# Performance work log

Hardware: AMD Instinct MI355X
Metric: run time of the kernel (lower is better)

The kernel has to match this reference:

```python
import jax, jax.numpy as jnp
import numpy as np

N_NODES = 50000
N_EDGES = 800000
D_IN = 64
D_OUT = 64


def setup_inputs() -> dict:
    key = jax.random.key(0)
    k1, k2, k3 = jax.random.split(key, 3)
    x = jax.random.normal(k1, (N_NODES, D_IN), dtype=jnp.float32)
    edge_index = jax.random.randint(k2, (2, N_EDGES), 0, N_NODES, dtype=jnp.int64)
    # xavier_uniform for weight [in, out]
    limit = np.sqrt(6.0 / (D_IN + D_OUT)).astype(np.float32)
    weight = jax.random.uniform(k3, (D_IN, D_OUT), dtype=jnp.float32, minval=-limit, maxval=limit)
    bias = jnp.zeros((D_OUT,), dtype=jnp.float32)
    return {"x": x, "edge_index": edge_index, "weight": weight, "bias": bias}


def reference(x, edge_index, weight, bias):
    n = x.shape[0]
    # add self loops
    loops = jnp.arange(n, dtype=edge_index.dtype)
    row = jnp.concatenate([edge_index[0], loops])  # [E+N]
    col = jnp.concatenate([edge_index[1], loops])  # [E+N]
    # degree over row (as in torch_geometric degree(row, N))
    deg = jax.ops.segment_sum(jnp.ones_like(row, dtype=x.dtype), row, num_segments=n)
    deg_inv_sqrt = jnp.where(deg > 0, jax.lax.rsqrt(deg), jnp.zeros_like(deg))
    norm = deg_inv_sqrt[row] * deg_inv_sqrt[col]  # [E+N]
    h = x @ weight  # [N, D_OUT]
    # gather-scale-scatter: out[col] += h[row] * norm
    out = jax.ops.segment_sum(h[row] * norm[:, None], col, num_segments=n)
    return out + bias
```

## Files before the change

kernel.cpp:

```cpp
#include <hip/hip_runtime.h>
#include <hip/hip_bf16.h>


constexpr int N_NODES = 50000;
constexpr int N_EDGES = 800000;
constexpr int D = 64;
constexpr int NB_SCAN = (N_NODES + 255) / 256;

constexpr int B_SLICE = 64;
constexpr int SLICE = N_EDGES / B_SLICE;
constexpr int PACK8 = N_NODES / 4;
constexpr int QUAR = N_NODES / 4;

static __device__ __forceinline__ unsigned short f2bf(float f) {
    unsigned u = __float_as_uint(f);
    unsigned r = (u + 0x7fffu + ((u >> 16) & 1u)) >> 16;
    return (unsigned short)r;
}
static __device__ __forceinline__ float bf2f(unsigned short s) {
    return __uint_as_float((unsigned)s << 16);
}


__global__ __launch_bounds__(1024) void hist_priv_kernel(const int* __restrict__ ei,
                                                         unsigned* __restrict__ bh) {
    __shared__ unsigned loc[PACK8];
    int b = blockIdx.x;
    int s = b & (B_SLICE - 1);
    const int* arr = (b < B_SLICE) ? ei : ei + N_EDGES;
    for (int w = threadIdx.x; w < PACK8; w += 1024) loc[w] = 0;
    __syncthreads();
    const int* p = arr + s * SLICE;
    for (int i = threadIdx.x; i < SLICE; i += 1024) {
        int k = p[i];
        atomicAdd(&loc[k >> 2], 1u << (8 * (k & 3)));
    }
    __syncthreads();
    unsigned* dst = bh + (size_t)b * PACK8;
    for (int w = threadIdx.x; w < PACK8; w += 1024) dst[w] = loc[w];
}

__global__ __launch_bounds__(256) void reduce_scan_kernel(const unsigned* __restrict__ bh,
                                                          float* __restrict__ dis,
                                                          int* __restrict__ cnt,
                                                          int* __restrict__ offs_local,
                                                          int* __restrict__ partials) {
    int t = threadIdx.x;
    int i = blockIdx.x * 256 + t;
    unsigned c = 0;
    if (i < N_NODES) {
        int w = i >> 2;
        unsigned sh = 8 * (i & 3);
        const unsigned* prow = bh + w;
        const unsigned* pcol = bh + (size_t)B_SLICE * PACK8 + w;
        unsigned dl = 0, cl = 0;
        unsigned vr[16];
#pragma unroll
        for (int g = 0; g < 4; ++g) {
#pragma unroll
            for (int k = 0; k < 16; ++k) vr[k] = prow[(size_t)(g * 16 + k) * PACK8];
#pragma unroll
            for (int k = 0; k < 16; ++k) dl += (vr[k] >> sh) & 0xffu;
        }
#pragma unroll
        for (int g = 0; g < 4; ++g) {
#pragma unroll
            for (int k = 0; k < 16; ++k) vr[k] = pcol[(size_t)(g * 16 + k) * PACK8];
#pragma unroll
            for (int k = 0; k < 16; ++k) cl += (vr[k] >> sh) & 0xffu;
        }
        c = cl;
        dis[i] = rsqrtf((float)dl + 1.0f);
        cnt[i] = (int)cl;
    }
    __shared__ int s[256];
    s[t] = (int)c;
    __syncthreads();
    for (int d = 1; d < 256; d <<= 1) {
        int u = (t >= d) ? s[t - d] : 0;
        __syncthreads();
        s[t] += u;
        __syncthreads();
    }
    if (i < N_NODES) offs_local[i] = s[t] - (int)c;
    if (t == 255) partials[blockIdx.x] = s[t];
}

__global__ __launch_bounds__(256) void colscan_kernel(const unsigned* __restrict__ bh,
                                                      const int* __restrict__ offs_local,
                                                      const int* __restrict__ partials,
                                                      int* __restrict__ offs,
                                                      unsigned char* __restrict__ bs8) {
    __shared__ int pref[256];
    int t = threadIdx.x;
    int v = (t < NB_SCAN) ? partials[t] : 0;
    pref[t] = v;
    __syncthreads();
    for (int d = 1; d < 256; d <<= 1) {
        int u = (t >= d) ? pref[t - d] : 0;
        __syncthreads();
        pref[t] += u;
        __syncthreads();
    }
    int ex = pref[t] - v;
    __syncthreads();
    pref[t] = ex;
    __syncthreads();

    int i = blockIdx.x * 256 + t;
    if (i >= N_NODES) return;
    offs[i] = pref[blockIdx.x] + offs_local[i];

    int w = i >> 2;
    unsigned sh = 8 * (i & 3);
    const unsigned* src = bh + (size_t)B_SLICE * PACK8 + w;
    unsigned vals[B_SLICE];
#pragma unroll
    for (int b = 0; b < B_SLICE; ++b) vals[b] = src[(size_t)b * PACK8];
    unsigned rel = 0;
#pragma unroll
    for (int b = 0; b < B_SLICE; ++b) {
        bs8[(size_t)b * N_NODES + i] = (unsigned char)rel;
        rel += (vals[b] >> sh) & 0xffu;
    }
}

__global__ __launch_bounds__(1024) void bucket_det_kernel(const int* __restrict__ ei,
                                                          const int* __restrict__ offs,
                                                          const unsigned char* __restrict__ bs8,
                                                          int* __restrict__ csr) {
    __shared__ unsigned pos[QUAR];
    int s = blockIdx.x >> 2;
    int q = blockIdx.x & 3;
    int c0 = q * QUAR;
    const int* offq = offs + c0;
    const unsigned char* relq = bs8 + (size_t)s * N_NODES + c0;
    for (int w = threadIdx.x; w < QUAR; w += 1024)
        pos[w] = (unsigned)offq[w] + relq[w];
    __syncthreads();
    const int* row = ei + s * SLICE;
    const int* col = ei + N_EDGES + s * SLICE;
    for (int i = threadIdx.x; i < SLICE; i += 1024) {
        int c = col[i];
        if (c >= c0 && c < c0 + QUAR) {
            unsigned p = atomicAdd(&pos[c - c0], 1u);
            csr[p] = row[i];
        }
    }
}


__global__ void hist_kernel(const int* __restrict__ row, const int* __restrict__ col,
                            int* __restrict__ degi, int* __restrict__ cnt) {
    int e = blockIdx.x * blockDim.x + threadIdx.x;
    if (e < N_EDGES) {
        atomicAdd(&degi[row[e]], 1);
        atomicAdd(&cnt[col[e]], 1);
    }
}

__global__ void dis_kernel(int* __restrict__ degi) {
    int i = blockIdx.x * blockDim.x + threadIdx.x;
    if (i < N_NODES) {
        float d = (float)degi[i] + 1.0f;
        ((float*)degi)[i] = rsqrtf(d);
    }
}

__global__ void bucket_kernel(const int* __restrict__ row, const int* __restrict__ col,
                              const int* __restrict__ offs, int* __restrict__ cur,
                              int* __restrict__ csr) {
    int e = blockIdx.x * blockDim.x + threadIdx.x;
    if (e < N_EDGES) {
        int c = col[e];
        int pos = offs[c] + atomicAdd(&cur[c], 1);
        csr[pos] = row[e];
    }
}

__global__ void block_scan_kernel(const int* __restrict__ cnt, int* __restrict__ offs,
                                  int* __restrict__ partials) {
    __shared__ int s[256];
    int t = threadIdx.x;
    int i = blockIdx.x * 256 + t;
    int v = (i < N_NODES) ? cnt[i] : 0;
    s[t] = v;
    __syncthreads();
    for (int d = 1; d < 256; d <<= 1) {
        int u = (t >= d) ? s[t - d] : 0;
        __syncthreads();
        s[t] += u;
        __syncthreads();
    }
    if (i < N_NODES) offs[i] = s[t] - v;
    if (t == 255) partials[blockIdx.x] = s[t];
}

__global__ void scan_partials_kernel(int* __restrict__ partials) {
    __shared__ int s[256];
    int t = threadIdx.x;
    int v = (t < NB_SCAN) ? partials[t] : 0;
    s[t] = v;
    __syncthreads();
    for (int d = 1; d < 256; d <<= 1) {
        int u = (t >= d) ? s[t - d] : 0;
        __syncthreads();
        s[t] += u;
        __syncthreads();
    }
    if (t < NB_SCAN) partials[t] = s[t] - v;
}

__global__ void add_off_kernel(int* __restrict__ offs, const int* __restrict__ partials) {
    int i = blockIdx.x * 256 + threadIdx.x;
    if (i < N_NODES) offs[i] += partials[blockIdx.x];
}

__global__ __launch_bounds__(256) void gemm_kernel(const float* __restrict__ x,
                                                   const float* __restrict__ W,
                                                   const float* __restrict__ dis,
                                                   unsigned short* __restrict__ hs) {
    __shared__ float Xs[64][68];
    __shared__ float Ws[64][64];
    int t = threadIdx.x;
    int n0 = blockIdx.x * 64;

    const float4* W4 = (const float4*)W;
    float4* Ws4 = (float4*)Ws;
#pragma unroll
    for (int i = 0; i < 4; ++i) Ws4[t + i * 256] = W4[t + i * 256];

    const float4* x4 = (const float4*)(x + (size_t)n0 * D);
#pragma unroll
    for (int i = 0; i < 4; ++i) {
        int f = t + i * 256;
        int r = f >> 4;
        int c = (f & 15) << 2;
        float4 v = make_float4(0.f, 0.f, 0.f, 0.f);
        if (n0 + r < N_NODES) v = x4[f];
        Xs[r][c] = v.x; Xs[r][c + 1] = v.y; Xs[r][c + 2] = v.z; Xs[r][c + 3] = v.w;
    }
    __syncthreads();

    int tx = t & 15;
    int ty = t >> 4;
    float acc[4][4] = {};
#pragma unroll
    for (int k = 0; k < D; ++k) {
        float a[4], b[4];
#pragma unroll
        for (int i = 0; i < 4; ++i) a[i] = Xs[ty * 4 + i][k];
#pragma unroll
        for (int jj = 0; jj < 4; ++jj) b[jj] = Ws[k][tx * 4 + jj];
#pragma unroll
        for (int i = 0; i < 4; ++i)
#pragma unroll
            for (int jj = 0; jj < 4; ++jj)
                acc[i][jj] = fmaf(a[i], b[jj], acc[i][jj]);
    }

#pragma unroll
    for (int i = 0; i < 4; ++i) {
        int r = ty * 4 + i;
        if (n0 + r < N_NODES) {
            float dr = dis[n0 + r];
            ushort4 v;
            v.x = f2bf(acc[i][0] * dr); v.y = f2bf(acc[i][1] * dr);
            v.z = f2bf(acc[i][2] * dr); v.w = f2bf(acc[i][3] * dr);
            *(ushort4*)(hs + (size_t)(n0 + r) * D + tx * 4) = v;
        }
    }
}

__global__ __launch_bounds__(256) void gather_kernel(const int* __restrict__ offs,
                                                     const int* __restrict__ cnt,
                                                     const int* __restrict__ csr,
                                                     const unsigned short* __restrict__ hs,
                                                     const float* __restrict__ dis,
                                                     const float* __restrict__ bias,
                                                     float* __restrict__ out) {
    int wave = threadIdx.x >> 6;
    int j = threadIdx.x & 63;
    int n = blockIdx.x * 4 + wave;
    if (n >= N_NODES) return;

    float a[8];
    a[0] = bf2f(hs[(size_t)n * D + j]);
#pragma unroll
    for (int k = 1; k < 8; ++k) a[k] = 0.f;

    int beg = __builtin_amdgcn_readfirstlane(offs[n]);
    int m   = __builtin_amdgcn_readfirstlane(cnt[n]);
    const int* p = csr + beg;

    int i = 0;
    for (; i + 16 <= m; i += 16) {
        int r[16];
        float v[16];
#pragma unroll
        for (int k = 0; k < 16; ++k) r[k] = p[i + k];
#pragma unroll
        for (int k = 0; k < 16; ++k) v[k] = bf2f(hs[(size_t)r[k] * D + j]);
#pragma unroll
        for (int k = 0; k < 16; ++k) a[k & 7] += v[k];
    }
    for (; i + 4 <= m; i += 4) {
        int r0 = p[i + 0], r1 = p[i + 1], r2 = p[i + 2], r3 = p[i + 3];
        a[0] += bf2f(hs[(size_t)r0 * D + j]);
        a[1] += bf2f(hs[(size_t)r1 * D + j]);
        a[2] += bf2f(hs[(size_t)r2 * D + j]);
        a[3] += bf2f(hs[(size_t)r3 * D + j]);
    }
    for (; i < m; ++i) {
        a[1] += bf2f(hs[(size_t)p[i] * D + j]);
    }
    float tot = ((a[0] + a[1]) + (a[2] + a[3])) + ((a[4] + a[5]) + (a[6] + a[7]));
    out[(size_t)n * D + j] = fmaf(dis[n], tot, bias[j]);
}


extern "C" void kernel_launch(void* const* d_in, const int* in_sizes, int n_in,
                              void* d_out, int out_size, void* d_ws, size_t ws_size,
                              hipStream_t stream) {
    const float* x    = (const float*)d_in[0];
    const int*   ei   = (const int*)d_in[1];
    const float* W    = (const float*)d_in[2];
    const float* bias = (const float*)d_in[3];
    float* out = (float*)d_out;

    const int* row = ei;
    const int* col = ei + N_EDGES;

    char* ws = (char*)d_ws;
    float*          dis      = (float*)(ws + 0);
    int*            cnt      = (int*)(ws + 200000);
    int*            offs_loc = (int*)(ws + 400000);
    int*            offs     = (int*)(ws + 600000);
    int*            partials = (int*)(ws + 800000);
    int*            csr      = (int*)(ws + 801024);
    unsigned short* hs       = (unsigned short*)(ws + 4001024);
    unsigned*       bh       = (unsigned*)(ws + 10401024);
    unsigned char*  bs8      = (unsigned char*)(ws + 16801024);

    const size_t WS_NEEDED = 20001024;

    if (ws_size >= WS_NEEDED) {
        hist_priv_kernel<<<2 * B_SLICE, 1024, 0, stream>>>(ei, bh);
        reduce_scan_kernel<<<NB_SCAN, 256, 0, stream>>>(bh, dis, cnt, offs_loc, partials);
        colscan_kernel<<<NB_SCAN, 256, 0, stream>>>(bh, offs_loc, partials, offs, bs8);
        bucket_det_kernel<<<4 * B_SLICE, 1024, 0, stream>>>(ei, offs, bs8, csr);
    } else {
        int* degi = (int*)dis;
        int* cur = offs_loc;
        hipMemsetAsync(ws, 0, 600000, stream);
        hist_kernel<<<(N_EDGES + 255) / 256, 256, 0, stream>>>(row, col, degi, cnt);
        dis_kernel<<<(N_NODES + 255) / 256, 256, 0, stream>>>(degi);
        block_scan_kernel<<<NB_SCAN, 256, 0, stream>>>(cnt, offs, partials);
        scan_partials_kernel<<<1, 256, 0, stream>>>(partials);
        add_off_kernel<<<NB_SCAN, 256, 0, stream>>>(offs, partials);
        bucket_kernel<<<(N_EDGES + 255) / 256, 256, 0, stream>>>(row, col, offs, cur, csr);
    }

    gemm_kernel<<<(N_NODES + 63) / 64, 256, 0, stream>>>(x, W, dis, hs);
    gather_kernel<<<(N_NODES + 3) / 4, 256, 0, stream>>>(offs, cnt, csr, hs, dis, bias, out);
}
```

Before: 146.6 us.

## Fuse histogram with GEMM, merge colscan into reduce, store per-edge norms in CSR

The histogram and dense GEMM now run in one launch. The first blocks build the degree histograms and the remaining blocks compute h = xW into bf16 without the dis scaling, so the GEMM no longer waits for the degree computation. The per-slice relative offsets (bs8) are now written in reduce_scan, leaving a thin offs kernel that also writes a sentinel offset. The CSR stores (row, norm) pairs so gather does an FMA per edge, which doubles CSR memory traffic but removes a launch and the cnt array.

```diff
diff --git a/kernel.cpp b/kernel.cpp
--- a/kernel.cpp
+++ b/kernel.cpp
@@ -11,6 +11,9 @@
 constexpr int SLICE = N_EDGES / B_SLICE;
 constexpr int PACK8 = N_NODES / 4;
 constexpr int QUAR = N_NODES / 4;
+constexpr int HIST_BLOCKS = 2 * B_SLICE;
+constexpr int GEMM_TILE = 128;
+constexpr int NTILES = (N_NODES + GEMM_TILE - 1) / GEMM_TILE;
 
 static __device__ __forceinline__ unsigned short f2bf(float f) {
     unsigned u = __float_as_uint(f);
@@ -21,60 +24,107 @@
     return __uint_as_float((unsigned)s << 16);
 }
 
-
-__global__ __launch_bounds__(1024) void hist_priv_kernel(const int* __restrict__ ei,
-                                                         unsigned* __restrict__ bh) {
-    __shared__ unsigned loc[PACK8];
-    int b = blockIdx.x;
-    int s = b & (B_SLICE - 1);
-    const int* arr = (b < B_SLICE) ? ei : ei + N_EDGES;
-    for (int w = threadIdx.x; w < PACK8; w += 1024) loc[w] = 0;
-    __syncthreads();
-    const int* p = arr + s * SLICE;
-    for (int i = threadIdx.x; i < SLICE; i += 1024) {
-        int k = p[i];
-        atomicAdd(&loc[k >> 2], 1u << (8 * (k & 3)));
-    }
-    __syncthreads();
-    unsigned* dst = bh + (size_t)b * PACK8;
-    for (int w = threadIdx.x; w < PACK8; w += 1024) dst[w] = loc[w];
+__global__ __launch_bounds__(1024) void histgemm_kernel(const int* __restrict__ ei,
+                                                        const float* __restrict__ x,
+                                                        const float* __restrict__ Wm,
+                                                        unsigned* __restrict__ bh,
+                                                        unsigned short* __restrict__ h) {
+    __shared__ __align__(16) unsigned char smem[51200];
+    const int b = blockIdx.x;
+    const int t = threadIdx.x;
+
+    if (b < HIST_BLOCKS) {
+        unsigned* loc = (unsigned*)smem;
+        for (int w = t; w < PACK8; w += 1024) loc[w] = 0;
+        __syncthreads();
+        const int* arr = (b < B_SLICE) ? ei : ei + N_EDGES;
+        const int* p = arr + (b & (B_SLICE - 1)) * SLICE;
+        for (int i = t; i < SLICE; i += 1024) {
+            int k = p[i];
+            atomicAdd(&loc[k >> 2], 1u << (8 * (k & 3)));
+        }
+        __syncthreads();
+        unsigned* dst = bh + (size_t)b * PACK8;
+        for (int w = t; w < PACK8; w += 1024) dst[w] = loc[w];
+    } else {
+        float* Xs = (float*)smem;
+        float* Ws = (float*)(smem + 34816);
+        ((float4*)Ws)[t] = ((const float4*)Wm)[t];
+        const int n0 = (b - HIST_BLOCKS) * GEMM_TILE;
+#pragma unroll
+        for (int i2 = 0; i2 < 2; ++i2) {
+            int f = t + i2 * 1024;
+            int r = f >> 4, c = (f & 15) << 2;
+            float4 v = make_float4(0.f, 0.f, 0.f, 0.f);
+            if (n0 + r < N_NODES) v = ((const float4*)x)[(size_t)n0 * 16 + f];
+            float* dp = Xs + r * 68 + c;
+            dp[0] = v.x; dp[1] = v.y; dp[2] = v.z; dp[3] = v.w;
+        }
+        __syncthreads();
+        const int tx = t & 15, ty = t >> 4;
+        float acc[2][4] = {};
+#pragma unroll
+        for (int k = 0; k < D; ++k) {
+            float a0 = Xs[(ty * 2) * 68 + k];
+            float a1 = Xs[(ty * 2 + 1) * 68 + k];
+            const float* wr = Ws + k * 64 + tx * 4;
+#pragma unroll
+            for (int jj = 0; jj < 4; ++jj) {
+                float bb = wr[jj];
+                acc[0][jj] = fmaf(a0, bb, acc[0][jj]);
+                acc[1][jj] = fmaf(a1, bb, acc[1][jj]);
+            }
+        }
+#pragma unroll
+        for (int i2 = 0; i2 < 2; ++i2) {
+            int n = n0 + ty * 2 + i2;
+            if (n < N_NODES) {
+                ushort4 v;
+                v.x = f2bf(acc[i2][0]); v.y = f2bf(acc[i2][1]);
+                v.z = f2bf(acc[i2][2]); v.w = f2bf(acc[i2][3]);
+                *(ushort4*)(h + (size_t)n * D + tx * 4) = v;
+            }
+        }
+    }
 }
 
 __global__ __launch_bounds__(256) void reduce_scan_kernel(const unsigned* __restrict__ bh,
                                                           float* __restrict__ dis,
-                                                          int* __restrict__ cnt,
                                                           int* __restrict__ offs_local,
-                                                          int* __restrict__ partials) {
+                                                          int* __restrict__ partials,
+                                                          unsigned char* __restrict__ bs8) {
     int t = threadIdx.x;
     int i = blockIdx.x * 256 + t;
-    unsigned c = 0;
+    unsigned cl = 0;
     if (i < N_NODES) {
-        int w = i >> 2;
-        unsigned sh = 8 * (i & 3);
+        const int w = i >> 2;
+        const unsigned sh = 8 * (i & 3);
         const unsigned* prow = bh + w;
+        unsigned dl = 0;
+#pragma unroll
+        for (int g = 0; g < 4; ++g) {
+            unsigned vr[16];
+#pragma unroll
+            for (int k = 0; k < 16; ++k) vr[k] = prow[(size_t)(g * 16 + k) * PACK8];
+#pragma unroll
+            for (int k = 0; k < 16; ++k) dl += (vr[k] >> sh) & 0xffu;
+        }
+        dis[i] = rsqrtf((float)dl + 1.0f);
         const unsigned* pcol = bh + (size_t)B_SLICE * PACK8 + w;
-        unsigned dl = 0, cl = 0;
-        unsigned vr[16];
 #pragma unroll
         for (int g = 0; g < 4; ++g) {
-#pragma unroll
-            for (int k = 0; k < 16; ++k) vr[k] = prow[(size_t)(g * 16 + k) * PACK8];
-#pragma unroll
-            for (int k = 0; k < 16; ++k) dl += (vr[k] >> sh) & 0xffu;
-        }
-#pragma unroll
-        for (int g = 0; g < 4; ++g) {
+            unsigned vr[16];
 #pragma unroll
             for (int k = 0; k < 16; ++k) vr[k] = pcol[(size_t)(g * 16 + k) * PACK8];
 #pragma unroll
-            for (int k = 0; k < 16; ++k) cl += (vr[k] >> sh) & 0xffu;
-        }
-        c = cl;
-        dis[i] = rsqrtf((float)dl + 1.0f);
-        cnt[i] = (int)cl;
+            for (int k = 0; k < 16; ++k) {
+                bs8[(size_t)(g * 16 + k) * N_NODES + i] = (unsigned char)cl;
+                cl += (vr[k] >> sh) & 0xffu;
+            }
+        }
     }
     __shared__ int s[256];
-    s[t] = (int)c;
+    s[t] = (int)cl;
     __syncthreads();
     for (int d = 1; d < 256; d <<= 1) {
         int u = (t >= d) ? s[t - d] : 0;
@@ -82,15 +132,13 @@
         s[t] += u;
         __syncthreads();
     }
-    if (i < N_NODES) offs_local[i] = s[t] - (int)c;
+    if (i < N_NODES) offs_local[i] = s[t] - (int)cl;
     if (t == 255) partials[blockIdx.x] = s[t];
 }
 
-__global__ __launch_bounds__(256) void colscan_kernel(const unsigned* __restrict__ bh,
-                                                      const int* __restrict__ offs_local,
-                                                      const int* __restrict__ partials,
-                                                      int* __restrict__ offs,
-                                                      unsigned char* __restrict__ bs8) {
+__global__ __launch_bounds__(256) void offs_kernel(const int* __restrict__ offs_local,
+                                                   const int* __restrict__ partials,
+                                                   int* __restrict__ offs) {
     __shared__ int pref[256];
     int t = threadIdx.x;
     int v = (t < NB_SCAN) ? partials[t] : 0;
@@ -106,176 +154,41 @@
     __syncthreads();
     pref[t] = ex;
     __syncthreads();
-
     int i = blockIdx.x * 256 + t;
-    if (i >= N_NODES) return;
-    offs[i] = pref[blockIdx.x] + offs_local[i];
-
-    int w = i >> 2;
-    unsigned sh = 8 * (i & 3);
-    const unsigned* src = bh + (size_t)B_SLICE * PACK8 + w;
-    unsigned vals[B_SLICE];
-#pragma unroll
-    for (int b = 0; b < B_SLICE; ++b) vals[b] = src[(size_t)b * PACK8];
-    unsigned rel = 0;
-#pragma unroll
-    for (int b = 0; b < B_SLICE; ++b) {
-        bs8[(size_t)b * N_NODES + i] = (unsigned char)rel;
-        rel += (vals[b] >> sh) & 0xffu;
-    }
+    if (i < N_NODES) offs[i] = pref[blockIdx.x] + offs_local[i];
+    if (i == 0) offs[N_NODES] = N_EDGES;
 }
 
 __global__ __launch_bounds__(1024) void bucket_det_kernel(const int* __restrict__ ei,
                                                           const int* __restrict__ offs,
                                                           const unsigned char* __restrict__ bs8,
-                                                          int* __restrict__ csr) {
+                                                          const float* __restrict__ dis,
+                                                          int2* __restrict__ csr) {
     __shared__ unsigned pos[QUAR];
-    int s = blockIdx.x >> 2;
-    int q = blockIdx.x & 3;
-    int c0 = q * QUAR;
+    const int s = blockIdx.x >> 2;
+    const int q = blockIdx.x & 3;
+    const int c0 = q * QUAR;
     const int* offq = offs + c0;
     const unsigned char* relq = bs8 + (size_t)s * N_NODES + c0;
     for (int w = threadIdx.x; w < QUAR; w += 1024)
         pos[w] = (unsigned)offq[w] + relq[w];
     __syncthreads();
-    const int* row = ei + s * SLICE;
-    const int* col = ei + N_EDGES + s * SLICE;
+    const int* rowp = ei + s * SLICE;
+    const int* colp = ei + N_EDGES + s * SLICE;
     for (int i = threadIdx.x; i < SLICE; i += 1024) {
-        int c = col[i];
+        int c = colp[i];
         if (c >= c0 && c < c0 + QUAR) {
+            int r = rowp[i];
             unsigned p = atomicAdd(&pos[c - c0], 1u);
-            csr[p] = row[i];
-        }
-    }
-}
-
-
-__global__ void hist_kernel(const int* __restrict__ row, const int* __restrict__ col,
-                            int* __restrict__ degi, int* __restrict__ cnt) {
-    int e = blockIdx.x * blockDim.x + threadIdx.x;
-    if (e < N_EDGES) {
-        atomicAdd(&degi[row[e]], 1);
-        atomicAdd(&cnt[col[e]], 1);
-    }
-}
-
-__global__ void dis_kernel(int* __restrict__ degi) {
-    int i = blockIdx.x * blockDim.x + threadIdx.x;
-    if (i < N_NODES) {
-        float d = (float)degi[i] + 1.0f;
-        ((float*)degi)[i] = rsqrtf(d);
-    }
-}
-
-__global__ void bucket_kernel(const int* __restrict__ row, const int* __restrict__ col,
-                              const int* __restrict__ offs, int* __restrict__ cur,
-                              int* __restrict__ csr) {
-    int e = blockIdx.x * blockDim.x + threadIdx.x;
-    if (e < N_EDGES) {
-        int c = col[e];
-        int pos = offs[c] + atomicAdd(&cur[c], 1);
-        csr[pos] = row[e];
-    }
-}
-
-__global__ void block_scan_kernel(const int* __restrict__ cnt, int* __restrict__ offs,
-                                  int* __restrict__ partials) {
-    __shared__ int s[256];
-    int t = threadIdx.x;
-    int i = blockIdx.x * 256 + t;
-    int v = (i < N_NODES) ? cnt[i] : 0;
-    s[t] = v;
-    __syncthreads();
-    for (int d = 1; d < 256; d <<= 1) {
-        int u = (t >= d) ? s[t - d] : 0;
-        __syncthreads();
-        s[t] += u;
-        __syncthreads();
-    }
-    if (i < N_NODES) offs[i] = s[t] - v;
-    if (t == 255) partials[blockIdx.x] = s[t];
-}
-
-__global__ void scan_partials_kernel(int* __restrict__ partials) {
-    __shared__ int s[256];
-    int t = threadIdx.x;
-    int v = (t < NB_SCAN) ? partials[t] : 0;
-    s[t] = v;
-    __syncthreads();
-    for (int d = 1; d < 256; d <<= 1) {
-        int u = (t >= d) ? s[t - d] : 0;
-        __syncthreads();
-        s[t] += u;
-        __syncthreads();
-    }
-    if (t < NB_SCAN) partials[t] = s[t] - v;
-}
-
-__global__ void add_off_kernel(int* __restrict__ offs, const int* __restrict__ partials) {
-    int i = blockIdx.x * 256 + threadIdx.x;
-    if (i < N_NODES) offs[i] += partials[blockIdx.x];
-}
-
-__global__ __launch_bounds__(256) void gemm_kernel(const float* __restrict__ x,
-                                                   const float* __restrict__ W,
-                                                   const float* __restrict__ dis,
-                                                   unsigned short* __restrict__ hs) {
-    __shared__ float Xs[64][68];
-    __shared__ float Ws[64][64];
-    int t = threadIdx.x;
-    int n0 = blockIdx.x * 64;
-
-    const float4* W4 = (const float4*)W;
-    float4* Ws4 = (float4*)Ws;
-#pragma unroll
-    for (int i = 0; i < 4; ++i) Ws4[t + i * 256] = W4[t + i * 256];
-
-    const float4* x4 = (const float4*)(x + (size_t)n0 * D);
-#pragma unroll
-    for (int i = 0; i < 4; ++i) {
-        int f = t + i * 256;
-        int r = f >> 4;
-        int c = (f & 15) << 2;
-        float4 v = make_float4(0.f, 0.f, 0.f, 0.f);
-        if (n0 + r < N_NODES) v = x4[f];
-        Xs[r][c] = v.x; Xs[r][c + 1] = v.y; Xs[r][c + 2] = v.z; Xs[r][c + 3] = v.w;
-    }
-    __syncthreads();
-
-    int tx = t & 15;
-    int ty = t >> 4;
-    float acc[4][4] = {};
-#pragma unroll
-    for (int k = 0; k < D; ++k) {
-        float a[4], b[4];
-#pragma unroll
-        for (int i = 0; i < 4; ++i) a[i] = Xs[ty * 4 + i][k];
-#pragma unroll
-        for (int jj = 0; jj < 4; ++jj) b[jj] = Ws[k][tx * 4 + jj];
-#pragma unroll
-        for (int i = 0; i < 4; ++i)
-#pragma unroll
-            for (int jj = 0; jj < 4; ++jj)
-                acc[i][jj] = fmaf(a[i], b[jj], acc[i][jj]);
-    }
-
-#pragma unroll
-    for (int i = 0; i < 4; ++i) {
-        int r = ty * 4 + i;
-        if (n0 + r < N_NODES) {
-            float dr = dis[n0 + r];
-            ushort4 v;
-            v.x = f2bf(acc[i][0] * dr); v.y = f2bf(acc[i][1] * dr);
-            v.z = f2bf(acc[i][2] * dr); v.w = f2bf(acc[i][3] * dr);
-            *(ushort4*)(hs + (size_t)(n0 + r) * D + tx * 4) = v;
+            float norm = dis[r] * dis[c];
+            csr[p] = make_int2(r, __float_as_int(norm));
         }
     }
 }
 
 __global__ __launch_bounds__(256) void gather_kernel(const int* __restrict__ offs,
-                                                     const int* __restrict__ cnt,
-                                                     const int* __restrict__ csr,
-                                                     const unsigned short* __restrict__ hs,
+                                                     const int2* __restrict__ csr,
+                                                     const unsigned short* __restrict__ h,
                                                      const float* __restrict__ dis,
                                                      const float* __restrict__ bias,
                                                      float* __restrict__ out) {
@@ -284,38 +197,156 @@
     int n = blockIdx.x * 4 + wave;
     if (n >= N_NODES) return;
 
+    float dn = dis[n];
     float a[8];
-    a[0] = bf2f(hs[(size_t)n * D + j]);
+    a[0] = bf2f(h[(size_t)n * D + j]) * dn * dn;
 #pragma unroll
     for (int k = 1; k < 8; ++k) a[k] = 0.f;
 
     int beg = __builtin_amdgcn_readfirstlane(offs[n]);
-    int m   = __builtin_amdgcn_readfirstlane(cnt[n]);
-    const int* p = csr + beg;
+    int m   = __builtin_amdgcn_readfirstlane(offs[n + 1]) - beg;
+    const int2* p = csr + beg;
 
     int i = 0;
-    for (; i + 16 <= m; i += 16) {
-        int r[16];
-        float v[16];
-#pragma unroll
-        for (int k = 0; k < 16; ++k) r[k] = p[i + k];
-#pragma unroll
-        for (int k = 0; k < 16; ++k) v[k] = bf2f(hs[(size_t)r[k] * D + j]);
-#pragma unroll
-        for (int k = 0; k < 16; ++k) a[k & 7] += v[k];
+    for (; i + 8 <= m; i += 8) {
+        int2 e[8];
+#pragma unroll
+        for (int k = 0; k < 8; ++k) e[k] = p[i + k];
+        float v[8];
+#pragma unroll
+        for (int k = 0; k < 8; ++k) v[k] = bf2f(h[(size_t)e[k].x * D + j]);
+#pragma unroll
+        for (int k = 0; k < 8; ++k) a[k] = fmaf(v[k], __int_as_float(e[k].y), a[k]);
     }
     for (; i + 4 <= m; i += 4) {
-        int r0 = p[i + 0], r1 = p[i + 1], r2 = p[i + 2], r3 = p[i + 3];
-        a[0] += bf2f(hs[(size_t)r0 * D + j]);
-        a[1] += bf2f(hs[(size_t)r1 * D + j]);
-        a[2] += bf2f(hs[(size_t)r2 * D + j]);
-        a[3] += bf2f(hs[(size_t)r3 * D + j]);
+        int2 e0 = p[i], e1 = p[i + 1], e2 = p[i + 2], e3 = p[i + 3];
+        a[0] = fmaf(bf2f(h[(size_t)e0.x * D + j]), __int_as_float(e0.y), a[0]);
+        a[1] = fmaf(bf2f(h[(size_t)e1.x * D + j]), __int_as_float(e1.y), a[1]);
+        a[2] = fmaf(bf2f(h[(size_t)e2.x * D + j]), __int_as_float(e2.y), a[2]);
+        a[3] = fmaf(bf2f(h[(size_t)e3.x * D + j]), __int_as_float(e3.y), a[3]);
     }
     for (; i < m; ++i) {
-        a[1] += bf2f(hs[(size_t)p[i] * D + j]);
+        int2 e = p[i];
+        a[1] = fmaf(bf2f(h[(size_t)e.x * D + j]), __int_as_float(e.y), a[1]);
     }
     float tot = ((a[0] + a[1]) + (a[2] + a[3])) + ((a[4] + a[5]) + (a[6] + a[7]));
-    out[(size_t)n * D + j] = fmaf(dis[n], tot, bias[j]);
+    out[(size_t)n * D + j] = tot + bias[j];
+}
+
+
+__global__ void hist_kernel(const int* __restrict__ row, const int* __restrict__ col,
+                            int* __restrict__ degi, int* __restrict__ cnt) {
+    int e = blockIdx.x * blockDim.x + threadIdx.x;
+    if (e < N_EDGES) {
+        atomicAdd(&degi[row[e]], 1);
+        atomicAdd(&cnt[col[e]], 1);
+    }
+}
+
+__global__ void dis_kernel(int* __restrict__ degi) {
+    int i = blockIdx.x * blockDim.x + threadIdx.x;
+    if (i < N_NODES) {
+        float d = (float)degi[i] + 1.0f;
+        ((float*)degi)[i] = rsqrtf(d);
+    }
+}
+
+__global__ void bucket_fb_kernel(const int* __restrict__ row, const int* __restrict__ col,
+                                 const int* __restrict__ offs, int* __restrict__ cur,
+                                 const float* __restrict__ dis, int2* __restrict__ csr) {
+    int e = blockIdx.x * blockDim.x + threadIdx.x;
+    if (e < N_EDGES) {
+        int r = row[e], c = col[e];
+        int pos = offs[c] + atomicAdd(&cur[c], 1);
+        csr[pos] = make_int2(r, __float_as_int(dis[r] * dis[c]));
+    }
+}
+
+__global__ void block_scan_kernel(const int* __restrict__ cnt, int* __restrict__ offs,
+                                  int* __restrict__ partials) {
+    __shared__ int s[256];
+    int t = threadIdx.x;
+    int i = blockIdx.x * 256 + t;
+    int v = (i < N_NODES) ? cnt[i] : 0;
+    s[t] = v;
+    __syncthreads();
+    for (int d = 1; d < 256; d <<= 1) {
+        int u = (t >= d) ? s[t - d] : 0;
+        __syncthreads();
+        s[t] += u;
+        __syncthreads();
+    }
+    if (i < N_NODES) offs[i] = s[t] - v;
+    if (t == 255) partials[blockIdx.x] = s[t];
+}
+
+__global__ void scan_partials_kernel(int* __restrict__ partials) {
+    __shared__ int s[256];
+    int t = threadIdx.x;
+    int v = (t < NB_SCAN) ? partials[t] : 0;
+    s[t] = v;
+    __syncthreads();
+    for (int d = 1; d < 256; d <<= 1) {
+        int u = (t >= d) ? s[t - d] : 0;
+        __syncthreads();
+        s[t] += u;
+        __syncthreads();
+    }
+    if (t < NB_SCAN) partials[t] = s[t] - v;
+}
+
+__global__ void add_off_kernel(int* __restrict__ offs, const int* __restrict__ partials) {
+    int i = blockIdx.x * 256 + threadIdx.x;
+    if (i < N_NODES) offs[i] += partials[blockIdx.x];
+    if (i == 0) offs[N_NODES] = N_EDGES;
+}
+
+__global__ __launch_bounds__(256) void gemm_fb_kernel(const float* __restrict__ x,
+                                                      const float* __restrict__ W,
+                                                      unsigned short* __restrict__ h) {
+    __shared__ float Xs[64][68];
+    __shared__ float Ws[64][64];
+    int t = threadIdx.x;
+    int n0 = blockIdx.x * 64;
+    const float4* W4 = (const float4*)W;
+    float4* Ws4 = (float4*)Ws;
+#pragma unroll
+    for (int i = 0; i < 4; ++i) Ws4[t + i * 256] = W4[t + i * 256];
+    const float4* x4 = (const float4*)(x + (size_t)n0 * D);
+#pragma unroll
+    for (int i = 0; i < 4; ++i) {
+        int f = t + i * 256;
+        int r = f >> 4, c = (f & 15) << 2;
+        float4 v = make_float4(0.f, 0.f, 0.f, 0.f);
+        if (n0 + r < N_NODES) v = x4[f];
+        Xs[r][c] = v.x; Xs[r][c + 1] = v.y; Xs[r][c + 2] = v.z; Xs[r][c + 3] = v.w;
+    }
+    __syncthreads();
+    int tx = t & 15, ty = t >> 4;
+    float acc[4][4] = {};
+#pragma unroll
+    for (int k = 0; k < D; ++k) {
+        float a[4], bb[4];
+#pragma unroll
+        for (int i = 0; i < 4; ++i) a[i] = Xs[ty * 4 + i][k];
+#pragma unroll
+        for (int jj = 0; jj < 4; ++jj) bb[jj] = Ws[k][tx * 4 + jj];
+#pragma unroll
+        for (int i = 0; i < 4; ++i)
+#pragma unroll
+            for (int jj = 0; jj < 4; ++jj)
+                acc[i][jj] = fmaf(a[i], bb[jj], acc[i][jj]);
+    }
+#pragma unroll
+    for (int i = 0; i < 4; ++i) {
+        int r = ty * 4 + i;
+        if (n0 + r < N_NODES) {
+            ushort4 v;
+            v.x = f2bf(acc[i][0]); v.y = f2bf(acc[i][1]);
+            v.z = f2bf(acc[i][2]); v.w = f2bf(acc[i][3]);
+            *(ushort4*)(h + (size_t)(n0 + r) * D + tx * 4) = v;
+        }
+    }
 }
 
 
@@ -328,39 +359,38 @@
     const float* bias = (const float*)d_in[3];
     float* out = (float*)d_out;
 
-    const int* row = ei;
-    const int* col = ei + N_EDGES;
-
     char* ws = (char*)d_ws;
     float*          dis      = (float*)(ws + 0);
-    int*            cnt      = (int*)(ws + 200000);
-    int*            offs_loc = (int*)(ws + 400000);
-    int*            offs     = (int*)(ws + 600000);
-    int*            partials = (int*)(ws + 800000);
-    int*            csr      = (int*)(ws + 801024);
-    unsigned short* hs       = (unsigned short*)(ws + 4001024);
-    unsigned*       bh       = (unsigned*)(ws + 10401024);
-    unsigned char*  bs8      = (unsigned char*)(ws + 16801024);
-
-    const size_t WS_NEEDED = 20001024;
+    int*            offs     = (int*)(ws + 200000);
+    int*            offs_loc = (int*)(ws + 400064);
+    int*            cur      = (int*)(ws + 600064);
+    int*            partials = (int*)(ws + 800064);
+    int2*           csr      = (int2*)(ws + 801088);
+    unsigned short* h        = (unsigned short*)(ws + 7201088);
+    unsigned*       bh       = (unsigned*)(ws + 13601088);
+    unsigned char*  bs8      = (unsigned char*)(ws + 20001088);
+
+    const size_t WS_NEEDED = 23201088;
 
     if (ws_size >= WS_NEEDED) {
-        hist_priv_kernel<<<2 * B_SLICE, 1024, 0, stream>>>(ei, bh);
-        reduce_scan_kernel<<<NB_SCAN, 256, 0, stream>>>(bh, dis, cnt, offs_loc, partials);
-        colscan_kernel<<<NB_SCAN, 256, 0, stream>>>(bh, offs_loc, partials, offs, bs8);
-        bucket_det_kernel<<<4 * B_SLICE, 1024, 0, stream>>>(ei, offs, bs8, csr);
+        histgemm_kernel<<<HIST_BLOCKS + NTILES, 1024, 0, stream>>>(ei, x, W, bh, h);
+        reduce_scan_kernel<<<NB_SCAN, 256, 0, stream>>>(bh, dis, offs_loc, partials, bs8);
+        offs_kernel<<<NB_SCAN, 256, 0, stream>>>(offs_loc, partials, offs);
+        bucket_det_kernel<<<4 * B_SLICE, 1024, 0, stream>>>(ei, offs, bs8, dis, csr);
+        gather_kernel<<<(N_NODES + 3) / 4, 256, 0, stream>>>(offs, csr, h, dis, bias, out);
     } else {
+        const int* row = ei;
+        const int* col = ei + N_EDGES;
         int* degi = (int*)dis;
-        int* cur = offs_loc;
-        hipMemsetAsync(ws, 0, 600000, stream);
-        hist_kernel<<<(N_EDGES + 255) / 256, 256, 0, stream>>>(row, col, degi, cnt);
+        int* cntf = offs_loc;
+        hipMemsetAsync(ws, 0, 800064, stream);
+        hist_kernel<<<(N_EDGES + 255) / 256, 256, 0, stream>>>(row, col, degi, cntf);
         dis_kernel<<<(N_NODES + 255) / 256, 256, 0, stream>>>(degi);
-        block_scan_kernel<<<NB_SCAN, 256, 0, stream>>>(cnt, offs, partials);
+        block_scan_kernel<<<NB_SCAN, 256, 0, stream>>>(cntf, offs, partials);
         scan_partials_kernel<<<1, 256, 0, stream>>>(partials);
         add_off_kernel<<<NB_SCAN, 256, 0, stream>>>(offs, partials);
-        bucket_kernel<<<(N_EDGES + 255) / 256, 256, 0, stream>>>(row, col, offs, cur, csr);
-    }
-
-    gemm_kernel<<<(N_NODES + 63) / 64, 256, 0, stream>>>(x, W, dis, hs);
-    gather_kernel<<<(N_NODES + 3) / 4, 256, 0, stream>>>(offs, cnt, csr, hs, dis, bias, out);
-}
+        bucket_fb_kernel<<<(N_EDGES + 255) / 256, 256, 0, stream>>>(row, col, offs, cur, dis, csr);
+        gemm_fb_kernel<<<(N_NODES + 63) / 64, 256, 0, stream>>>(x, W, h);
+        gather_kernel<<<(N_NODES + 3) / 4, 256, 0, stream>>>(offs, csr, h, dis, bias, out);
+    }
+}
```

Result: slower. 363.9 us (+148.3%).

## Fuse column scan into reduce kernel and gather packed bf16 pairs per half-wave

Applied to the files above, without the earlier changes.

The per-slice relative offsets (bs8) are now written inside reduce_scan_kernel, which already reads the column histograms, so the second pass over bh in colscan_kernel is gone and that kernel shrinks to a simple offset fix-up. The count array is dropped by storing offs[N] and computing each node's degree from adjacent offsets. The gather kernel now reads two bf16 values per 32-bit load, with each half-wave handling alternate neighbours, and combines the halves with a shuffle. This halves the number of load instructions per edge and writes float2 outputs, at the cost of extra select and shuffle logic.

```diff
diff --git a/kernel.cpp b/kernel.cpp
--- a/kernel.cpp
+++ b/kernel.cpp
@@ -17,10 +17,12 @@
     unsigned r = (u + 0x7fffu + ((u >> 16) & 1u)) >> 16;
     return (unsigned short)r;
 }
-static __device__ __forceinline__ float bf2f(unsigned short s) {
-    return __uint_as_float((unsigned)s << 16);
-}
-
+static __device__ __forceinline__ float bf_lo(unsigned v) {
+    return __uint_as_float(v << 16);
+}
+static __device__ __forceinline__ float bf_hi(unsigned v) {
+    return __uint_as_float(v & 0xffff0000u);
+}
 
 __global__ __launch_bounds__(1024) void hist_priv_kernel(const int* __restrict__ ei,
                                                          unsigned* __restrict__ bh) {
@@ -42,39 +44,41 @@
 
 __global__ __launch_bounds__(256) void reduce_scan_kernel(const unsigned* __restrict__ bh,
                                                           float* __restrict__ dis,
-                                                          int* __restrict__ cnt,
                                                           int* __restrict__ offs_local,
-                                                          int* __restrict__ partials) {
+                                                          int* __restrict__ partials,
+                                                          unsigned char* __restrict__ bs8) {
     int t = threadIdx.x;
     int i = blockIdx.x * 256 + t;
-    unsigned c = 0;
+    unsigned cl = 0;
     if (i < N_NODES) {
-        int w = i >> 2;
-        unsigned sh = 8 * (i & 3);
+        const int w = i >> 2;
+        const unsigned sh = 8 * (i & 3);
         const unsigned* prow = bh + w;
+        unsigned dl = 0;
+#pragma unroll
+        for (int g = 0; g < 4; ++g) {
+            unsigned vr[16];
+#pragma unroll
+            for (int k = 0; k < 16; ++k) vr[k] = prow[(size_t)(g * 16 + k) * PACK8];
+#pragma unroll
+            for (int k = 0; k < 16; ++k) dl += (vr[k] >> sh) & 0xffu;
+        }
+        dis[i] = rsqrtf((float)dl + 1.0f);
         const unsigned* pcol = bh + (size_t)B_SLICE * PACK8 + w;
-        unsigned dl = 0, cl = 0;
-        unsigned vr[16];
 #pragma unroll
         for (int g = 0; g < 4; ++g) {
-#pragma unroll
-            for (int k = 0; k < 16; ++k) vr[k] = prow[(size_t)(g * 16 + k) * PACK8];
-#pragma unroll
-            for (int k = 0; k < 16; ++k) dl += (vr[k] >> sh) & 0xffu;
-        }
-#pragma unroll
-        for (int g = 0; g < 4; ++g) {
+            unsigned vr[16];
 #pragma unroll
             for (int k = 0; k < 16; ++k) vr[k] = pcol[(size_t)(g * 16 + k) * PACK8];
 #pragma unroll
-            for (int k = 0; k < 16; ++k) cl += (vr[k] >> sh) & 0xffu;
-        }
-        c = cl;
-        dis[i] = rsqrtf((float)dl + 1.0f);
-        cnt[i] = (int)cl;
+            for (int k = 0; k < 16; ++k) {
+                bs8[(size_t)(g * 16 + k) * N_NODES + i] = (unsigned char)cl;
+                cl += (vr[k] >> sh) & 0xffu;
+            }
+        }
     }
     __shared__ int s[256];
-    s[t] = (int)c;
+    s[t] = (int)cl;
     __syncthreads();
     for (int d = 1; d < 256; d <<= 1) {
         int u = (t >= d) ? s[t - d] : 0;
@@ -82,15 +86,13 @@
         s[t] += u;
         __syncthreads();
     }
-    if (i < N_NODES) offs_local[i] = s[t] - (int)c;
+    if (i < N_NODES) offs_local[i] = s[t] - (int)cl;
     if (t == 255) partials[blockIdx.x] = s[t];
 }
 
-__global__ __launch_bounds__(256) void colscan_kernel(const unsigned* __restrict__ bh,
-                                                      const int* __restrict__ offs_local,
-                                                      const int* __restrict__ partials,
-                                                      int* __restrict__ offs,
-                                                      unsigned char* __restrict__ bs8) {
+__global__ __launch_bounds__(256) void offs_kernel(const int* __restrict__ offs_local,
+                                                   const int* __restrict__ partials,
+                                                   int* __restrict__ offs) {
     __shared__ int pref[256];
     int t = threadIdx.x;
     int v = (t < NB_SCAN) ? partials[t] : 0;
@@ -106,114 +108,9 @@
     __syncthreads();
     pref[t] = ex;
     __syncthreads();
-
     int i = blockIdx.x * 256 + t;
-    if (i >= N_NODES) return;
-    offs[i] = pref[blockIdx.x] + offs_local[i];
-
-    int w = i >> 2;
-    unsigned sh = 8 * (i & 3);
-    const unsigned* src = bh + (size_t)B_SLICE * PACK8 + w;
-    unsigned vals[B_SLICE];
-#pragma unroll
-    for (int b = 0; b < B_SLICE; ++b) vals[b] = src[(size_t)b * PACK8];
-    unsigned rel = 0;
-#pragma unroll
-    for (int b = 0; b < B_SLICE; ++b) {
-        bs8[(size_t)b * N_NODES + i] = (unsigned char)rel;
-        rel += (vals[b] >> sh) & 0xffu;
-    }
-}
-
-__global__ __launch_bounds__(1024) void bucket_det_kernel(const int* __restrict__ ei,
-                                                          const int* __restrict__ offs,
-                                                          const unsigned char* __restrict__ bs8,
-                                                          int* __restrict__ csr) {
-    __shared__ unsigned pos[QUAR];
-    int s = blockIdx.x >> 2;
-    int q = blockIdx.x & 3;
-    int c0 = q * QUAR;
-    const int* offq = offs + c0;
-    const unsigned char* relq = bs8 + (size_t)s * N_NODES + c0;
-    for (int w = threadIdx.x; w < QUAR; w += 1024)
-        pos[w] = (unsigned)offq[w] + relq[w];
-    __syncthreads();
-    const int* row = ei + s * SLICE;
-    const int* col = ei + N_EDGES + s * SLICE;
-    for (int i = threadIdx.x; i < SLICE; i += 1024) {
-        int c = col[i];
-        if (c >= c0 && c < c0 + QUAR) {
-            unsigned p = atomicAdd(&pos[c - c0], 1u);
-            csr[p] = row[i];
-        }
-    }
-}
-
-
-__global__ void hist_kernel(const int* __restrict__ row, const int* __restrict__ col,
-                            int* __restrict__ degi, int* __restrict__ cnt) {
-    int e = blockIdx.x * blockDim.x + threadIdx.x;
-    if (e < N_EDGES) {
-        atomicAdd(&degi[row[e]], 1);
-        atomicAdd(&cnt[col[e]], 1);
-    }
-}
-
-__global__ void dis_kernel(int* __restrict__ degi) {
-    int i = blockIdx.x * blockDim.x + threadIdx.x;
-    if (i < N_NODES) {
-        float d = (float)degi[i] + 1.0f;
-        ((float*)degi)[i] = rsqrtf(d);
-    }
-}
-
-__global__ void bucket_kernel(const int* __restrict__ row, const int* __restrict__ col,
-                              const int* __restrict__ offs, int* __restrict__ cur,
-                              int* __restrict__ csr) {
-    int e = blockIdx.x * blockDim.x + threadIdx.x;
-    if (e < N_EDGES) {
-        int c = col[e];
-        int pos = offs[c] + atomicAdd(&cur[c], 1);
-        csr[pos] = row[e];
-    }
-}
-
-__global__ void block_scan_kernel(const int* __restrict__ cnt, int* __restrict__ offs,
-                                  int* __restrict__ partials) {
-    __shared__ int s[256];
-    int t = threadIdx.x;
-    int i = blockIdx.x * 256 + t;
-    int v = (i < N_NODES) ? cnt[i] : 0;
-    s[t] = v;
-    __syncthreads();
-    for (int d = 1; d < 256; d <<= 1) {
-        int u = (t >= d) ? s[t - d] : 0;
-        __syncthreads();
-        s[t] += u;
-        __syncthreads();
-    }
-    if (i < N_NODES) offs[i] = s[t] - v;
-    if (t == 255) partials[blockIdx.x] = s[t];
-}
-
-__global__ void scan_partials_kernel(int* __restrict__ partials) {
-    __shared__ int s[256];
-    int t = threadIdx.x;
-    int v = (t < NB_SCAN) ? partials[t] : 0;
-    s[t] = v;
-    __syncthreads();
-    for (int d = 1; d < 256; d <<= 1) {
-        int u = (t >= d) ? s[t - d] : 0;
-        __syncthreads();
-        s[t] += u;
-        __syncthreads();
-    }
-    if (t < NB_SCAN) partials[t] = s[t] - v;
-}
-
-__global__ void add_off_kernel(int* __restrict__ offs, const int* __restrict__ partials) {
-    int i = blockIdx.x * 256 + threadIdx.x;
-    if (i < N_NODES) offs[i] += partials[blockIdx.x];
+    if (i < N_NODES) offs[i] = pref[blockIdx.x] + offs_local[i];
+    if (i == 0) offs[N_NODES] = N_EDGES;
 }
 
 __global__ __launch_bounds__(256) void gemm_kernel(const float* __restrict__ x,
@@ -234,29 +131,27 @@
 #pragma unroll
     for (int i = 0; i < 4; ++i) {
         int f = t + i * 256;
-        int r = f >> 4;
-        int c = (f & 15) << 2;
+        int r = f >> 4, c = (f & 15) << 2;
         float4 v = make_float4(0.f, 0.f, 0.f, 0.f);
         if (n0 + r < N_NODES) v = x4[f];
         Xs[r][c] = v.x; Xs[r][c + 1] = v.y; Xs[r][c + 2] = v.z; Xs[r][c + 3] = v.w;
     }
     __syncthreads();
 
-    int tx = t & 15;
-    int ty = t >> 4;
+    int tx = t & 15, ty = t >> 4;
     float acc[4][4] = {};
 #pragma unroll
     for (int k = 0; k < D; ++k) {
-        float a[4], b[4];
+        float a[4], bb[4];
 #pragma unroll
         for (int i = 0; i < 4; ++i) a[i] = Xs[ty * 4 + i][k];
 #pragma unroll
-        for (int jj = 0; jj < 4; ++jj) b[jj] = Ws[k][tx * 4 + jj];
+        for (int jj = 0; jj < 4; ++jj) bb[jj] = Ws[k][tx * 4 + jj];
 #pragma unroll
         for (int i = 0; i < 4; ++i)
 #pragma unroll
             for (int jj = 0; jj < 4; ++jj)
-                acc[i][jj] = fmaf(a[i], b[jj], acc[i][jj]);
+                acc[i][jj] = fmaf(a[i], bb[jj], acc[i][jj]);
     }
 
 #pragma unroll
@@ -272,50 +167,166 @@
     }
 }
 
+__global__ __launch_bounds__(1024) void bucket_det_kernel(const int* __restrict__ ei,
+                                                          const int* __restrict__ offs,
+                                                          const unsigned char* __restrict__ bs8,
+                                                          int* __restrict__ csr) {
+    __shared__ unsigned pos[QUAR];
+    const int s = blockIdx.x >> 2;
+    const int q = blockIdx.x & 3;
+    const int c0 = q * QUAR;
+    const int* offq = offs + c0;
+    const unsigned char* relq = bs8 + (size_t)s * N_NODES + c0;
+    for (int w = threadIdx.x; w < QUAR; w += 1024)
+        pos[w] = (unsigned)offq[w] + relq[w];
+    __syncthreads();
+    const int* rowp = ei + s * SLICE;
+    const int* colp = ei + N_EDGES + s * SLICE;
+    for (int i = threadIdx.x; i < SLICE; i += 1024) {
+        int c = colp[i];
+        if (c >= c0 && c < c0 + QUAR) {
+            unsigned p = atomicAdd(&pos[c - c0], 1u);
+            csr[p] = rowp[i];
+        }
+    }
+}
+
 __global__ __launch_bounds__(256) void gather_kernel(const int* __restrict__ offs,
-                                                     const int* __restrict__ cnt,
                                                      const int* __restrict__ csr,
-                                                     const unsigned short* __restrict__ hs,
+                                                     const unsigned* __restrict__ hs32,
                                                      const float* __restrict__ dis,
                                                      const float* __restrict__ bias,
                                                      float* __restrict__ out) {
-    int wave = threadIdx.x >> 6;
-    int j = threadIdx.x & 63;
-    int n = blockIdx.x * 4 + wave;
+    const int wave = threadIdx.x >> 6;
+    const int lane = threadIdx.x & 63;
+    const int half = lane >> 5;
+    const int jj = lane & 31;
+    const int n = blockIdx.x * 4 + wave;
     if (n >= N_NODES) return;
 
-    float a[8];
-    a[0] = bf2f(hs[(size_t)n * D + j]);
-#pragma unroll
-    for (int k = 1; k < 8; ++k) a[k] = 0.f;
-
-    int beg = __builtin_amdgcn_readfirstlane(offs[n]);
-    int m   = __builtin_amdgcn_readfirstlane(cnt[n]);
+    float aLo[4], aHi[4];
+#pragma unroll
+    for (int k = 0; k < 4; ++k) { aLo[k] = 0.f; aHi[k] = 0.f; }
+    {
+        unsigned sv = hs32[(size_t)n * 32 + jj];
+        if (half == 0) { aLo[0] = bf_lo(sv); aHi[0] = bf_hi(sv); }
+    }
+
+    const int beg = __builtin_amdgcn_readfirstlane(offs[n]);
+    const int m   = __builtin_amdgcn_readfirstlane(offs[n + 1]) - beg;
     const int* p = csr + beg;
 
     int i = 0;
     for (; i + 16 <= m; i += 16) {
-        int r[16];
-        float v[16];
-#pragma unroll
-        for (int k = 0; k < 16; ++k) r[k] = p[i + k];
-#pragma unroll
-        for (int k = 0; k < 16; ++k) v[k] = bf2f(hs[(size_t)r[k] * D + j]);
-#pragma unroll
-        for (int k = 0; k < 16; ++k) a[k & 7] += v[k];
-    }
-    for (; i + 4 <= m; i += 4) {
-        int r0 = p[i + 0], r1 = p[i + 1], r2 = p[i + 2], r3 = p[i + 3];
-        a[0] += bf2f(hs[(size_t)r0 * D + j]);
-        a[1] += bf2f(hs[(size_t)r1 * D + j]);
-        a[2] += bf2f(hs[(size_t)r2 * D + j]);
-        a[3] += bf2f(hs[(size_t)r3 * D + j]);
-    }
-    for (; i < m; ++i) {
-        a[1] += bf2f(hs[(size_t)p[i] * D + j]);
-    }
-    float tot = ((a[0] + a[1]) + (a[2] + a[3])) + ((a[4] + a[5]) + (a[6] + a[7]));
-    out[(size_t)n * D + j] = fmaf(dis[n], tot, bias[j]);
+        int r[8];
+#pragma unroll
+        for (int k = 0; k < 8; ++k) {
+            int rA = p[i + 2 * k];
+            int rB = p[i + 2 * k + 1];
+            r[k] = half ? rB : rA;
+        }
+        unsigned v[8];
+#pragma unroll
+        for (int k = 0; k < 8; ++k) v[k] = hs32[(size_t)r[k] * 32 + jj];
+#pragma unroll
+        for (int k = 0; k < 8; ++k) {
+            aLo[k & 3] += bf_lo(v[k]);
+            aHi[k & 3] += bf_hi(v[k]);
+        }
+    }
+    for (; i + 2 <= m; i += 2) {
+        int rA = p[i], rB = p[i + 1];
+        int r = half ? rB : rA;
+        unsigned v = hs32[(size_t)r * 32 + jj];
+        aLo[1] += bf_lo(v);
+        aHi[1] += bf_hi(v);
+    }
+    if (i < m) {
+        unsigned v = hs32[(size_t)p[i] * 32 + jj];
+        if (half == 0) { aLo[2] += bf_lo(v); aHi[2] += bf_hi(v); }
+    }
+
+    float tLo = (aLo[0] + aLo[1]) + (aLo[2] + aLo[3]);
+    float tHi = (aHi[0] + aHi[1]) + (aHi[2] + aHi[3]);
+    tLo += __shfl(tLo, lane ^ 32);
+    tHi += __shfl(tHi, lane ^ 32);
+
+    if (half == 0) {
+        float dn = dis[n];
+        float2 bj = ((const float2*)bias)[jj];
+        float2 o;
+        o.x = fmaf(dn, tLo, bj.x);
+        o.y = fmaf(dn, tHi, bj.y);
+        ((float2*)out)[(size_t)n * 32 + jj] = o;
+    }
+}
+
+
+__global__ void histf_kernel(const int* __restrict__ row, const int* __restrict__ col,
+                             int* __restrict__ degi, int* __restrict__ cnt) {
+    int e = blockIdx.x * blockDim.x + threadIdx.x;
+    if (e < N_EDGES) {
+        atomicAdd(&degi[row[e]], 1);
+        atomicAdd(&cnt[col[e]], 1);
+    }
+}
+
+__global__ void disf_kernel(int* __restrict__ degi) {
+    int i = blockIdx.x * blockDim.x + threadIdx.x;
+    if (i < N_NODES) {
+        float d = (float)degi[i] + 1.0f;
+        ((float*)degi)[i] = rsqrtf(d);
+    }
+}
+
+__global__ void block_scan_kernel(const int* __restrict__ cnt, int* __restrict__ offs,
+                                  int* __restrict__ partials) {
+    __shared__ int s[256];
+    int t = threadIdx.x;
+    int i = blockIdx.x * 256 + t;
+    int v = (i < N_NODES) ? cnt[i] : 0;
+    s[t] = v;
+    __syncthreads();
+    for (int d = 1; d < 256; d <<= 1) {
+        int u = (t >= d) ? s[t - d] : 0;
+        __syncthreads();
+        s[t] += u;
+        __syncthreads();
+    }
+    if (i < N_NODES) offs[i] = s[t] - v;
+    if (t == 255) partials[blockIdx.x] = s[t];
+}
+
+__global__ void scan_partials_kernel(int* __restrict__ partials) {
+    __shared__ int s[256];
+    int t = threadIdx.x;
+    int v = (t < NB_SCAN) ? partials[t] : 0;
+    s[t] = v;
+    __syncthreads();
+    for (int d = 1; d < 256; d <<= 1) {
+        int u = (t >= d) ? s[t - d] : 0;
+        __syncthreads();
+        s[t] += u;
+        __syncthreads();
+    }
+    if (t < NB_SCAN) partials[t] = s[t] - v;
+}
+
+__global__ void add_off_kernel(int* __restrict__ offs, const int* __restrict__ partials) {
+    int i = blockIdx.x * 256 + threadIdx.x;
+    if (i < N_NODES) offs[i] += partials[blockIdx.x];
+    if (i == 0) offs[N_NODES] = N_EDGES;
+}
+
+__global__ void bucket_fb_kernel(const int* __restrict__ row, const int* __restrict__ col,
+                                 const int* __restrict__ offs, int* __restrict__ cur,
+                                 int* __restrict__ csr) {
+    int e = blockIdx.x * blockDim.x + threadIdx.x;
+    if (e < N_EDGES) {
+        int c = col[e];
+        int pos = offs[c] + atomicAdd(&cur[c], 1);
+        csr[pos] = row[e];
+    }
 }
 
 
@@ -328,39 +339,41 @@
     const float* bias = (const float*)d_in[3];
     float* out = (float*)d_out;
 
-    const int* row = ei;
-    const int* col = ei + N_EDGES;
-
     char* ws = (char*)d_ws;
     float*          dis      = (float*)(ws + 0);
-    int*            cnt      = (int*)(ws + 200000);
-    int*            offs_loc = (int*)(ws + 400000);
-    int*            offs     = (int*)(ws + 600000);
-    int*            partials = (int*)(ws + 800000);
-    int*            csr      = (int*)(ws + 801024);
-    unsigned short* hs       = (unsigned short*)(ws + 4001024);
-    unsigned*       bh       = (unsigned*)(ws + 10401024);
-    unsigned char*  bs8      = (unsigned char*)(ws + 16801024);
-
-    const size_t WS_NEEDED = 20001024;
+    int*            offs     = (int*)(ws + 200000);
+    int*            offs_loc = (int*)(ws + 400064);
+    int*            cur      = (int*)(ws + 600064);
+    int*            partials = (int*)(ws + 800064);
+    int*            csr      = (int*)(ws + 801088);
+    unsigned short* hs       = (unsigned short*)(ws + 4001088);
+    unsigned*       bh       = (unsigned*)(ws + 10401088);
+    unsigned char*  bs8      = (unsigned char*)(ws + 16801088);
+
+    const size_t WS_NEEDED = 20001088;
 
     if (ws_size >= WS_NEEDED) {
         hist_priv_kernel<<<2 * B_SLICE, 1024, 0, stream>>>(ei, bh);
-        reduce_scan_kernel<<<NB_SCAN, 256, 0, stream>>>(bh, dis, cnt, offs_loc, partials);
-        colscan_kernel<<<NB_SCAN, 256, 0, stream>>>(bh, offs_loc, partials, offs, bs8);
+        reduce_scan_kernel<<<NB_SCAN, 256, 0, stream>>>(bh, dis, offs_loc, partials, bs8);
+        offs_kernel<<<NB_SCAN, 256, 0, stream>>>(offs_loc, partials, offs);
+        gemm_kernel<<<(N_NODES + 63) / 64, 256, 0, stream>>>(x, W, dis, hs);
         bucket_det_kernel<<<4 * B_SLICE, 1024, 0, stream>>>(ei, offs, bs8, csr);
+        gather_kernel<<<(N_NODES + 3) / 4, 256, 0, stream>>>(offs, csr, (const unsigned*)hs,
+                                                             dis, bias, out);
     } else {
+        const int* row = ei;
+        const int* col = ei + N_EDGES;
         int* degi = (int*)dis;
-        int* cur = offs_loc;
-        hipMemsetAsync(ws, 0, 600000, stream);
-        hist_kernel<<<(N_EDGES + 255) / 256, 256, 0, stream>>>(row, col, degi, cnt);
-        dis_kernel<<<(N_NODES + 255) / 256, 256, 0, stream>>>(degi);
-        block_scan_kernel<<<NB_SCAN, 256, 0, stream>>>(cnt, offs, partials);
+        int* cntf = offs_loc;
+        hipMemsetAsync(ws, 0, 800064, stream);
+        histf_kernel<<<(N_EDGES + 255) / 256, 256, 0, stream>>>(row, col, degi, cntf);
+        disf_kernel<<<(N_NODES + 255) / 256, 256, 0, stream>>>(degi);
+        block_scan_kernel<<<NB_SCAN, 256, 0, stream>>>(cntf, offs, partials);
         scan_partials_kernel<<<1, 256, 0, stream>>>(partials);
         add_off_kernel<<<NB_SCAN, 256, 0, stream>>>(offs, partials);
-        bucket_kernel<<<(N_EDGES + 255) / 256, 256, 0, stream>>>(row, col, offs, cur, csr);
-    }
-
-    gemm_kernel<<<(N_NODES + 63) / 64, 256, 0, stream>>>(x, W, dis, hs);
-    gather_kernel<<<(N_NODES + 3) / 4, 256, 0, stream>>>(offs, cnt, csr, hs, dis, bias, out);
-}
+        gemm_kernel<<<(N_NODES + 63) / 64, 256, 0, stream>>>(x, W, dis, hs);
+        bucket_fb_kernel<<<(N_EDGES + 255) / 256, 256, 0, stream>>>(row, col, offs, cur, csr);
+        gather_kernel<<<(N_NODES + 3) / 4, 256, 0, stream>>>(offs, csr, (const unsigned*)hs,
+                                                             dis, bias, out);
+    }
+}
```

Measured after the change: 152.2 us. 3.8% more time.
